# Kernel tuning notes

Hardware: AMD Instinct MI355X
Metric: run time of the kernel (lower is better)

The kernel has to match this reference:

```python
import jax, jax.numpy as jnp
import numpy as np
from math import ceil, sqrt

# Inner module: Linear(2048,4096)+ReLU, Linear(4096,4096)+ReLU, Linear(4096,2048)
D_IN, D_H, D_OUT = 2048, 4096, 2048
BATCH = 4096
# named_modules() order: each Linear yields weight then bias; ReLU skipped
SHAPES = [(D_H, D_IN), (D_H,), (D_H, D_H), (D_H,), (D_OUT, D_H), (D_OUT,)]
NUM_P = sum(int(np.prod(s)) for s in SHAPES)  # 33_566_720
SIZE_N = ceil(sqrt(NUM_P))                    # 5794
SIZE_M = ceil(1.0 * SIZE_N / 2)               # 2897 (compress = 1.0)


def setup_inputs() -> dict:
    key = jax.random.key(0)
    k1, k2, k3 = jax.random.split(key, 3)
    k = sqrt(12) / 2 * SIZE_M ** (-0.25)  # norm_V init bound
    V1 = jax.random.uniform(k1, (SIZE_N, SIZE_M), jnp.float32, -k, k)
    V2 = jax.random.uniform(k2, (SIZE_M, SIZE_N), jnp.float32, -k, k)
    x = jax.random.normal(k3, (BATCH, D_IN), jnp.float32)
    return {"x": x, "V1": V1, "V2": V2}


def _unpack(Vf):
    # scatter-copy: contiguous slices of flattened V -> weights/biases in traversal order
    params, i = [], 0
    for s in SHAPES:
        n = int(np.prod(s))
        params.append(Vf[i:i + n].reshape(s))
        i += n
    return params


def reference(x, V1, V2):
    # WandBtoV: low-rank reconstruction then per-element copy into weights (fused here)
    Vf = (V1 @ V2).reshape(-1)  # [SIZE_N*SIZE_N]; only first NUM_P elements used
    W1, b1, W2, b2, W3, b3 = _unpack(Vf)
    h = jax.nn.relu(x @ W1.T + b1)   # [B, D_H]
    h = jax.nn.relu(h @ W2.T + b2)   # [B, D_H]
    return h @ W3.T + b3             # [B, D_OUT]
```

## Files before the change

kernel.cpp:

```cpp
#include <hip/hip_runtime.h>
#include <stdint.h>

typedef __attribute__((ext_vector_type(8)))  __bf16 bf16x8;
typedef __attribute__((ext_vector_type(4)))  float  f32x4;
typedef __attribute__((ext_vector_type(16))) float  f32x16;
typedef unsigned short u16;
typedef __attribute__((ext_vector_type(8))) unsigned short u16x8;

#define GLOBAL_AS __attribute__((address_space(1)))
#define LDS_AS    __attribute__((address_space(3)))

__device__ __forceinline__ void load_lds16(const void* g, void* l) {
    __builtin_amdgcn_global_load_lds((const GLOBAL_AS void*)g, (LDS_AS void*)l, 16, 0, 0);
}

__device__ __forceinline__ u16 f2bf(float f) {
    union { float f; uint32_t u; } v; v.f = f;
    uint32_t r = v.u + 0x7FFFu + ((v.u >> 16) & 1u);
    return (u16)(r >> 16);
}
__device__ __forceinline__ float b2f(u16 b) {
    union { uint32_t u; float f; } v; v.u = ((uint32_t)b) << 16;
    return v.f;
}

__global__ void k_conv_pad(const float* __restrict__ in, u16* __restrict__ out,
                           int rIn, int cIn, int cOut, int total8) {
    int idx = blockIdx.x * blockDim.x + threadIdx.x;
    if (idx >= total8) return;
    int c8n = cOut >> 3;
    int r  = idx / c8n;
    int c0 = (idx - r * c8n) << 3;
    u16x8 o;
#pragma unroll
    for (int j = 0; j < 8; ++j) {
        int c = c0 + j;
        o[j] = (r < rIn && c < cIn) ? f2bf(in[(size_t)r * cIn + c]) : (u16)0;
    }
    *(u16x8*)(out + (size_t)r * cOut + c0) = o;
}

__global__ void k_transpose_conv(const float* __restrict__ in, u16* __restrict__ out,
                                 int kIn, int nIn, int kOut) {
    __shared__ float tile[32][33];
    int k0 = blockIdx.x * 32, n0 = blockIdx.y * 32;
    int tx = threadIdx.x, ty = threadIdx.y;
#pragma unroll
    for (int i = 0; i < 4; ++i) {
        int k = k0 + ty + i * 8, n = n0 + tx;
        tile[ty + i * 8][tx] = (k < kIn && n < nIn) ? in[(size_t)k * nIn + n] : 0.f;
    }
    __syncthreads();
#pragma unroll
    for (int i = 0; i < 4; ++i) {
        int n = n0 + ty + i * 8, k = k0 + tx;
        out[(size_t)n * kOut + k] = f2bf(tile[tx][ty + i * 8]);
    }
}

template <int MODE>
__global__ __launch_bounds__(256, 4) void k_gemm_bt(
    const u16* __restrict__ A, const u16* __restrict__ B,
    const u16* __restrict__ bias, void* __restrict__ Cv,
    int K, int ldc, int mReal, int nReal) {
    (void)bias;
    __shared__ __align__(16) char lds[32768];
    char* As = lds;
    char* Bs = lds + 16384;

    const int tid  = threadIdx.x;
    const int w    = tid >> 6, lane = tid & 63;
    const int l31  = lane & 31, hi = lane >> 5;
    const int wm   = (w & 1) * 64, wn = (w >> 1) * 64;
    const int bm   = blockIdx.y * 128, bn = blockIdx.x * 128;

    const int srcRow = tid >> 3;
    const int srcCol = (tid & 7) ^ (srcRow & 7);
    const u16* aSrc = A + (size_t)(bm + srcRow) * K + (srcCol << 3);
    const u16* bSrc = B + (size_t)(bn + srcRow) * K + (srcCol << 3);
    char* aDst = As + ((tid & ~63) << 4);
    char* bDst = Bs + ((tid & ~63) << 4);

    const int aRow0 = (wm + l31) * 128;
    const int aRow1 = (wm + 32 + l31) * 128;
    const int bRow0 = (wn + l31) * 128;
    const int bRow1 = (wn + 32 + l31) * 128;

    f32x16 acc[2][2];
#pragma unroll
    for (int i = 0; i < 2; ++i)
#pragma unroll
        for (int j = 0; j < 2; ++j) acc[i][j] = (f32x16)(0.f);

    for (int k0 = 0; k0 < K; k0 += 64) {
#pragma unroll
        for (int t = 0; t < 4; ++t) {
            load_lds16(aSrc + (size_t)(t * 32) * K, aDst + t * 4096);
            load_lds16(bSrc + (size_t)(t * 32) * K, bDst + t * 4096);
        }
        aSrc += 64; bSrc += 64;
        __syncthreads();
#pragma unroll
        for (int ks = 0; ks < 4; ++ks) {
            const int swz = (((ks * 2 + hi) ^ (l31 & 7)) << 4);
            bf16x8 af[2], bfr[2];
            af[0]  = *(const bf16x8*)(As + aRow0 + swz);
            af[1]  = *(const bf16x8*)(As + aRow1 + swz);
            bfr[0] = *(const bf16x8*)(Bs + bRow0 + swz);
            bfr[1] = *(const bf16x8*)(Bs + bRow1 + swz);
#pragma unroll
            for (int mi = 0; mi < 2; ++mi)
#pragma unroll
                for (int ni = 0; ni < 2; ++ni)
                    acc[mi][ni] = __builtin_amdgcn_mfma_f32_32x32x16_bf16(
                        af[mi], bfr[ni], acc[mi][ni], 0, 0, 0);
        }
        __syncthreads();
    }

    float bv[2];
    if (MODE >= 1) {
#pragma unroll
        for (int ni = 0; ni < 2; ++ni) bv[ni] = b2f(bias[bn + wn + ni * 32 + l31]);
    }
#pragma unroll
    for (int mi = 0; mi < 2; ++mi) {
#pragma unroll
        for (int reg = 0; reg < 16; ++reg) {
            int row = bm + wm + mi * 32 + (reg & 3) + 8 * (reg >> 2) + 4 * hi;
#pragma unroll
            for (int ni = 0; ni < 2; ++ni) {
                int col = bn + wn + ni * 32 + l31;
                float v = acc[mi][ni][reg];
                if (MODE == 0) {
                    if (row < mReal && col < nReal)
                        ((u16*)Cv)[(size_t)row * ldc + col] = f2bf(v);
                } else if (MODE == 1) {
                    v += bv[ni];
                    v = v > 0.f ? v : 0.f;
                    ((u16*)Cv)[(size_t)row * ldc + col] = f2bf(v);
                } else {
                    ((float*)Cv)[(size_t)row * ldc + col] = v + bv[ni];
                }
            }
        }
    }
}


#define BARRIER() do { asm volatile("" ::: "memory"); \
                       __builtin_amdgcn_s_barrier(); \
                       asm volatile("" ::: "memory"); } while (0)
#define LGKM0()   do { asm volatile("s_waitcnt lgkmcnt(0)" ::: "memory"); \
                       __builtin_amdgcn_sched_barrier(0); } while (0)
#define LGKM8()   do { asm volatile("s_waitcnt lgkmcnt(8)" ::: "memory"); \
                       __builtin_amdgcn_sched_barrier(0); } while (0)
#define VMCNT(n)  do { asm volatile("s_waitcnt vmcnt(" #n ")" ::: "memory"); \
                       __builtin_amdgcn_sched_barrier(0); } while (0)

#define STG_A(BUFB, H, KT) do { \
    load_lds16(aStage + (size_t)((H) * 128)      * K + (KT), lds + (BUFB) * 65536 + (H) * 16384 +        ldsW); \
    load_lds16(aStage + (size_t)((H) * 128 + 64) * K + (KT), lds + (BUFB) * 65536 + (H) * 16384 + 8192 + ldsW); \
} while (0)
#define STG_B(BUFB, H, KT) do { \
    load_lds16(bStage + (size_t)((H) * 128)      * K + (KT), lds + (BUFB) * 65536 + 32768 + (H) * 16384 +        ldsW); \
    load_lds16(bStage + (size_t)((H) * 128 + 64) * K + (KT), lds + (BUFB) * 65536 + 32768 + (H) * 16384 + 8192 + ldsW); \
} while (0)

#define RDA(BUFB, MH) do { \
    _Pragma("unroll") for (int m2 = 0; m2 < 4; ++m2) { \
        a[m2][0] = *(const bf16x8*)(lds + (BUFB) * 65536 + aWave + (MH) * 8192 + m2 * 2048 + laneF); \
        a[m2][1] = *(const bf16x8*)(lds + (BUFB) * 65536 + aWave + (MH) * 8192 + m2 * 2048 + (laneF ^ 64)); \
    } } while (0)
#define RDB(BUFB, NH, DST) do { \
    _Pragma("unroll") for (int n2 = 0; n2 < 2; ++n2) { \
        DST[n2][0] = *(const bf16x8*)(lds + (BUFB) * 65536 + bWave + (NH) * 4096 + n2 * 2048 + laneF); \
        DST[n2][1] = *(const bf16x8*)(lds + (BUFB) * 65536 + bWave + (NH) * 4096 + n2 * 2048 + (laneF ^ 64)); \
    } } while (0)

#define MM16(AA, BB, MH, NH) do { \
    __builtin_amdgcn_s_setprio(1); \
    _Pragma("unroll") for (int ks = 0; ks < 2; ++ks) \
    _Pragma("unroll") for (int n2 = 0; n2 < 2; ++n2) \
    _Pragma("unroll") for (int m2 = 0; m2 < 4; ++m2) \
        acc[(MH) * 4 + m2][(NH) * 2 + n2] = __builtin_amdgcn_mfma_f32_16x16x32_bf16( \
            AA[m2][ks], BB[n2][ks], acc[(MH) * 4 + m2][(NH) * 2 + n2], 0, 0, 0); \
    __builtin_amdgcn_s_setprio(0); \
} while (0)

template <int MODE>
__global__ __launch_bounds__(512, 2) void k_gemm8p(
    const u16* __restrict__ A, const u16* __restrict__ B,
    const u16* __restrict__ bias, void* __restrict__ Cv,
    int K, int ldc, int mReal, int nReal, int gx, int nTiles) {
    __shared__ __align__(16) char lds[131072];

    const int tid  = threadIdx.x;
    const int w    = tid >> 6, lane = tid & 63;
    const int wc   = w & 3, wr = w >> 2;
    const int l15  = lane & 15, lg4 = lane >> 4;

    const int nwg = (int)gridDim.x;
    const int q   = nwg >> 3, r = nwg & 7;
    const int xcd = (int)blockIdx.x & 7, lid = (int)blockIdx.x >> 3;
    const int wg0 = (xcd < r ? xcd * (q + 1) : r * (q + 1) + (xcd - r) * q) + lid;

    const int laneF = l15 * 128 + (((lane >> 4) ^ (lane & 7)) << 4);
    const int aWave = wr * 16384;
    const int bWave = 32768 + (wc >> 1) * 16384 + (wc & 1) * 8192;

    const int cOrig = (lane & 7) ^ ((lane >> 3) & 7);
    const int sRow  = w * 8 + (lane >> 3);
    const int ldsW  = w * 1024;

    const int nIt = K >> 7;

    for (int v = wg0; v < nTiles; v += (int)gridDim.x) {
        const int bm = (v / gx) * 256;
        const int bn = (v % gx) * 256;
        const u16* const aStage = A + (size_t)(bm + sRow) * K + cOrig * 8;
        const u16* const bStage = B + (size_t)(bn + sRow) * K + cOrig * 8;

        f32x4 acc[8][4];
#pragma unroll
        for (int i = 0; i < 8; ++i)
#pragma unroll
            for (int j = 0; j < 4; ++j) acc[i][j] = (f32x4)(0.f);

        bf16x8 a[4][2], b0[2][2], b1[2][2];

        STG_A(0, 0, 0);  STG_B(0, 0, 0);  STG_A(0, 1, 0);  STG_B(0, 1, 0);
        STG_B(1, 0, 64); STG_B(1, 1, 64);
        VMCNT(4);
        BARRIER();

#pragma unroll 1
        for (int it = 0; it < nIt; ++it) {
            const bool ok = (it + 1 < nIt);
            const size_t kT1 = (size_t)(2 * it + 1) * 64;
            const size_t kS  = (size_t)(2 * it + 2) * 64;
            RDA(0, 0); RDB(0, 0, b0); STG_A(1, 0, kT1);
            LGKM8(); BARRIER(); LGKM0(); MM16(a, b0, 0, 0); BARRIER();
            RDB(0, 1, b1); STG_A(1, 1, kT1);
            BARRIER(); LGKM0(); MM16(a, b1, 0, 1); BARRIER();
            RDA(0, 1); if (ok) { STG_B(0, 0, kS); }
            BARRIER(); LGKM0(); MM16(a, b1, 1, 1); BARRIER();
            if (ok) { STG_B(0, 1, kS); VMCNT(4); } else { VMCNT(0); }
            BARRIER(); MM16(a, b0, 1, 0); BARRIER();
            RDA(1, 0); RDB(1, 0, b0); if (ok) { STG_A(0, 0, kS); }
            LGKM8(); BARRIER(); LGKM0(); MM16(a, b0, 0, 0); BARRIER();
            RDB(1, 1, b1); if (ok) { STG_A(0, 1, kS); }
            BARRIER(); LGKM0(); MM16(a, b1, 0, 1); BARRIER();
            RDA(1, 1); if (ok) { STG_B(1, 0, kS + 64); }
            BARRIER(); LGKM0(); MM16(a, b1, 1, 1); BARRIER();
            if (ok) { STG_B(1, 1, kS + 64); VMCNT(4); }
            BARRIER(); MM16(a, b0, 1, 0); BARRIER();
        }

        float bv[4];
        if (MODE >= 1) {
#pragma unroll
            for (int ni = 0; ni < 4; ++ni) bv[ni] = b2f(bias[bn + wc * 64 + ni * 16 + l15]);
        }
#pragma unroll
        for (int mi = 0; mi < 8; ++mi) {
#pragma unroll
            for (int ni = 0; ni < 4; ++ni) {
#pragma unroll
                for (int rg = 0; rg < 4; ++rg) {
                    const int row = bm + wr * 128 + mi * 16 + lg4 * 4 + rg;
                    const int col = bn + wc * 64 + ni * 16 + l15;
                    float vv = acc[mi][ni][rg];
                    if (MODE == 0) {
                        if (row < mReal && col < nReal)
                            ((u16*)Cv)[(size_t)row * ldc + col] = f2bf(vv);
                    } else if (MODE == 1) {
                        vv += bv[ni];
                        vv = vv > 0.f ? vv : 0.f;
                        ((u16*)Cv)[(size_t)row * ldc + col] = f2bf(vv);
                    } else {
                        ((float*)Cv)[(size_t)row * ldc + col] = vv + bv[ni];
                    }
                }
            }
        }
    }
}

extern "C" void kernel_launch(void* const* d_in, const int* in_sizes, int n_in,
                              void* d_out, int out_size, void* d_ws, size_t ws_size,
                              hipStream_t stream) {
    (void)in_sizes; (void)n_in; (void)out_size; (void)ws_size;
    const float* x  = (const float*)d_in[0];
    const float* V1 = (const float*)d_in[1];
    const float* V2 = (const float*)d_in[2];

    char* ws = (char*)d_ws;
    u16* Vf   = (u16*)(ws);
    u16* V1b  = (u16*)(ws + 67141120);
    u16* V2bT = (u16*)(ws + 67141120 + 34668544);
    u16* Xb   = (u16*)(ws + 67141120 + 2 * 34668544);
    u16* H1   = V1b;
    u16* H2   = V2bT;

    k_conv_pad<<<8464, 256, 0, stream>>>(V1, V1b, 5794, 2897, 2944, 5888 * 2944 / 8);
    k_transpose_conv<<<dim3(92, 184), dim3(32, 8), 0, stream>>>(V2, V2bT, 2897, 5794, 2944);
    k_conv_pad<<<4096, 256, 0, stream>>>(x, Xb, 4096, 2048, 2048, 4096 * 2048 / 8);

    k_gemm8p<0><<<512, 512, 0, stream>>>(V1b, V2bT, nullptr, Vf,
                                         2944, 5794, 5794, 5794, 23, 529);
    k_gemm8p<1><<<256, 512, 0, stream>>>(Xb, Vf + 0, Vf + 8388608, H1,
                                         2048, 4096, 4096, 4096, 16, 256);
    k_gemm8p<1><<<256, 512, 0, stream>>>(H1, Vf + 8392704, Vf + 25169920, H2,
                                         4096, 4096, 4096, 4096, 16, 256);
    k_gemm_bt<2><<<dim3(16, 32), 256, 0, stream>>>(H2, Vf + 25174016, Vf + 33562624, d_out,
                                                   4096, 2048, 4096, 2048);
}
```

Measured before the change: 700.5 us.

## Double-buffer LDS fragment registers and reschedule GEMM main loop pipeline

Restructures the 256x256 bf16 MFMA main loop so A and B register fragments are double-buffered (aP/aQ, bP/bQ). LDS reads for the next sub-tile are issued before the current MFMA block, and partial lgkmcnt waits replace full waits. Global-to-LDS stage issue order is also rearranged, with one fewer barrier per sub-step. The goal is to hide LDS read latency behind MFMA work and cut synchronization stalls, at the cost of more VGPRs and tricky hazard ordering between LDS buffer reuse and async loads.

```diff
diff --git a/kernel.cpp b/kernel.cpp
--- a/kernel.cpp
+++ b/kernel.cpp
@@ -153,7 +153,11 @@
                        asm volatile("" ::: "memory"); } while (0)
 #define LGKM0()   do { asm volatile("s_waitcnt lgkmcnt(0)" ::: "memory"); \
                        __builtin_amdgcn_sched_barrier(0); } while (0)
+#define LGKM4()   do { asm volatile("s_waitcnt lgkmcnt(4)" ::: "memory"); \
+                       __builtin_amdgcn_sched_barrier(0); } while (0)
 #define LGKM8()   do { asm volatile("s_waitcnt lgkmcnt(8)" ::: "memory"); \
+                       __builtin_amdgcn_sched_barrier(0); } while (0)
+#define LGKM12()  do { asm volatile("s_waitcnt lgkmcnt(12)" ::: "memory"); \
                        __builtin_amdgcn_sched_barrier(0); } while (0)
 #define VMCNT(n)  do { asm volatile("s_waitcnt vmcnt(" #n ")" ::: "memory"); \
                        __builtin_amdgcn_sched_barrier(0); } while (0)
@@ -167,10 +171,10 @@
     load_lds16(bStage + (size_t)((H) * 128 + 64) * K + (KT), lds + (BUFB) * 65536 + 32768 + (H) * 16384 + 8192 + ldsW); \
 } while (0)
 
-#define RDA(BUFB, MH) do { \
+#define RDA(BUFB, MH, DST) do { \
     _Pragma("unroll") for (int m2 = 0; m2 < 4; ++m2) { \
-        a[m2][0] = *(const bf16x8*)(lds + (BUFB) * 65536 + aWave + (MH) * 8192 + m2 * 2048 + laneF); \
-        a[m2][1] = *(const bf16x8*)(lds + (BUFB) * 65536 + aWave + (MH) * 8192 + m2 * 2048 + (laneF ^ 64)); \
+        DST[m2][0] = *(const bf16x8*)(lds + (BUFB) * 65536 + aWave + (MH) * 8192 + m2 * 2048 + laneF); \
+        DST[m2][1] = *(const bf16x8*)(lds + (BUFB) * 65536 + aWave + (MH) * 8192 + m2 * 2048 + (laneF ^ 64)); \
     } } while (0)
 #define RDB(BUFB, NH, DST) do { \
     _Pragma("unroll") for (int n2 = 0; n2 < 2; ++n2) { \
@@ -227,34 +231,44 @@
 #pragma unroll
             for (int j = 0; j < 4; ++j) acc[i][j] = (f32x4)(0.f);
 
-        bf16x8 a[4][2], b0[2][2], b1[2][2];
-
-        STG_A(0, 0, 0);  STG_B(0, 0, 0);  STG_A(0, 1, 0);  STG_B(0, 1, 0);
-        STG_B(1, 0, 64); STG_B(1, 1, 64);
-        VMCNT(4);
+        bf16x8 aP[4][2], aQ[4][2], bP[2][2], bQ[2][2];
+
+        STG_A(0, 0, 0);  STG_A(0, 1, 0);  STG_B(0, 0, 0);  STG_B(0, 1, 0);
+        STG_A(1, 0, 64); STG_A(1, 1, 64); STG_B(1, 0, 64);
+        VMCNT(6);
         BARRIER();
+        RDA(0, 0, aP); RDB(0, 0, bP);
 
 #pragma unroll 1
         for (int it = 0; it < nIt; ++it) {
             const bool ok = (it + 1 < nIt);
             const size_t kT1 = (size_t)(2 * it + 1) * 64;
             const size_t kS  = (size_t)(2 * it + 2) * 64;
-            RDA(0, 0); RDB(0, 0, b0); STG_A(1, 0, kT1);
-            LGKM8(); BARRIER(); LGKM0(); MM16(a, b0, 0, 0); BARRIER();
-            RDB(0, 1, b1); STG_A(1, 1, kT1);
-            BARRIER(); LGKM0(); MM16(a, b1, 0, 1); BARRIER();
-            RDA(0, 1); if (ok) { STG_B(0, 0, kS); }
-            BARRIER(); LGKM0(); MM16(a, b1, 1, 1); BARRIER();
-            if (ok) { STG_B(0, 1, kS); VMCNT(4); } else { VMCNT(0); }
-            BARRIER(); MM16(a, b0, 1, 0); BARRIER();
-            RDA(1, 0); RDB(1, 0, b0); if (ok) { STG_A(0, 0, kS); }
-            LGKM8(); BARRIER(); LGKM0(); MM16(a, b0, 0, 0); BARRIER();
-            RDB(1, 1, b1); if (ok) { STG_A(0, 1, kS); }
-            BARRIER(); LGKM0(); MM16(a, b1, 0, 1); BARRIER();
-            RDA(1, 1); if (ok) { STG_B(1, 0, kS + 64); }
-            BARRIER(); LGKM0(); MM16(a, b1, 1, 1); BARRIER();
-            if (ok) { STG_B(1, 1, kS + 64); VMCNT(4); }
-            BARRIER(); MM16(a, b0, 1, 0); BARRIER();
+            STG_B(1, 1, kT1);
+            RDA(0, 1, aQ);
+            LGKM8(); MM16(aP, bP, 0, 0); BARRIER();
+            RDB(0, 1, bQ);
+            LGKM4(); MM16(aQ, bP, 1, 0); BARRIER();
+            if (ok) { STG_A(0, 0, kS); VMCNT(2); } else { VMCNT(0); }
+            LGKM0(); MM16(aQ, bQ, 1, 1); BARRIER();
+            if (ok) { STG_A(0, 1, kS); STG_B(0, 0, kS); }
+            RDA(1, 0, aQ); RDB(1, 0, bP);
+            LGKM12(); MM16(aP, bQ, 0, 1); BARRIER();
+            if (ok) { STG_B(0, 1, kS); }
+            RDA(1, 1, aP);
+            LGKM8(); MM16(aQ, bP, 0, 0); BARRIER();
+            RDB(1, 1, bQ);
+            LGKM4(); MM16(aP, bP, 1, 0); BARRIER();
+            if (ok) { STG_A(1, 0, kS + 64); VMCNT(2); }
+            LGKM0(); MM16(aP, bQ, 1, 1); BARRIER();
+            if (ok) {
+                STG_A(1, 1, kS + 64); STG_B(1, 0, kS + 64);
+                RDA(0, 0, aP); RDB(0, 0, bP);
+                LGKM12();
+            } else {
+                LGKM0();
+            }
+            MM16(aQ, bQ, 0, 1); BARRIER();
         }
 
         float bv[4];
```

After: 1.383 ms. 97.5% more time.
